# Performance work log

Hardware: AMD Instinct MI355X
Metric: run time of the kernel (lower is better)

Reference implementation:

```python
import jax, jax.numpy as jnp
import numpy as np

D_MODEL = 1024
H = 16
D_K = D_MODEL // H


def setup_inputs() -> dict:
    key = jax.random.key(0)
    ks = jax.random.split(key, 12)
    B, S = 4, 2048
    s = 1.0 / np.sqrt(D_MODEL)
    return {
        "Q": jax.random.normal(ks[0], (B, S, D_MODEL), jnp.float32),
        "K": jax.random.normal(ks[1], (B, S, D_MODEL), jnp.float32),
        "V": jax.random.normal(ks[2], (B, S, D_MODEL), jnp.float32),
        "attn_mask": jnp.ones((B, S), jnp.int32),
        "Wq": jax.random.normal(ks[3], (D_MODEL, D_MODEL), jnp.float32) * s,
        "bq": jax.random.normal(ks[4], (D_MODEL,), jnp.float32) * s,
        "Wk": jax.random.normal(ks[5], (D_MODEL, D_MODEL), jnp.float32) * s,
        "bk": jax.random.normal(ks[6], (D_MODEL,), jnp.float32) * s,
        "Wv": jax.random.normal(ks[7], (D_MODEL, D_MODEL), jnp.float32) * s,
        "bv": jax.random.normal(ks[8], (D_MODEL,), jnp.float32) * s,
        "Wo": jax.random.normal(ks[9], (D_MODEL, D_MODEL), jnp.float32) * s,
        "bo": jax.random.normal(ks[10], (D_MODEL,), jnp.float32) * s,
    }


def _split_heads(x):
    B, S, _ = x.shape
    return x.reshape(B, S, H, D_K).transpose(0, 2, 1, 3)  # (B,H,S,Dk)


def reference(Q, K, V, attn_mask, Wq, bq, Wk, bk, Wv, bv, Wo, bo):
    # Linear projections (torch Linear: x @ W.T + b)
    q = _split_heads(Q @ Wq.T + bq)
    k = _split_heads(K @ Wk.T + bk)
    v = _split_heads(V @ Wv.T + bv)
    scale = 1.0 / jnp.sqrt(jnp.asarray(D_K, q.dtype))
    scores = jnp.einsum("bhqd,bhkd->bhqk", q, k) * scale  # (B,H,S,S)
    # 2-D mask (B,S) broadcast over heads and query positions; 0 -> -inf
    mask = attn_mask[:, None, None, :]
    scores = jnp.where(mask == 0, -jnp.inf, scores)
    attn = jax.nn.softmax(scores, axis=-1)
    # dropout_proba = 0.0 -> identity
    x = jnp.einsum("bhqk,bhkd->bhqd", attn, v)
    B, _, S, _ = x.shape
    x = x.transpose(0, 2, 1, 3).reshape(B, S, D_MODEL)
    return x @ Wo.T + bo
```

## Files before the change

### kernel.cpp

```cpp
#include <hip/hip_runtime.h>
#include <stdint.h>

typedef unsigned short u16;
typedef __attribute__((ext_vector_type(8))) unsigned short u16x8;
typedef __attribute__((ext_vector_type(4))) unsigned short u16x4;
typedef __attribute__((ext_vector_type(2))) __fp16 h16x2;
typedef __attribute__((ext_vector_type(4))) _Float16 f16x4;
typedef __attribute__((ext_vector_type(8))) _Float16 f16x8;
typedef __attribute__((ext_vector_type(4))) float f32x4;

#define MFMA16F16(a,b,c)  __builtin_amdgcn_mfma_f32_16x16x16f16((a),(b),(c),0,0,0)
#define MFMA32F16(a,b,c)  __builtin_amdgcn_mfma_f32_16x16x32_f16((a),(b),(c),0,0,0)

__device__ __forceinline__ f32x4 f4zero() {
    f32x4 z; z[0]=0.f; z[1]=0.f; z[2]=0.f; z[3]=0.f; return z;
}
__device__ __forceinline__ u16x8 cvth8(float4 a, float4 b) {
    union { h16x2 h[4]; u16x8 u; } U;
    U.h[0] = __builtin_amdgcn_cvt_pkrtz(a.x, a.y);
    U.h[1] = __builtin_amdgcn_cvt_pkrtz(a.z, a.w);
    U.h[2] = __builtin_amdgcn_cvt_pkrtz(b.x, b.y);
    U.h[3] = __builtin_amdgcn_cvt_pkrtz(b.z, b.w);
    return U.u;
}

#define GLDS(gp, lp) __builtin_amdgcn_global_load_lds( \
    (const __attribute__((address_space(1))) void*)(gp), \
    (__attribute__((address_space(3))) void*)(lp), 16, 0, 0)

#define QSC 0.1803368801111601f

__global__ __launch_bounds__(256) void conv_all(
    const float* __restrict__ w0, const float* __restrict__ w1,
    const float* __restrict__ w2, const float* __restrict__ w3,
    const float* __restrict__ x0, const float* __restrict__ x1,
    const float* __restrict__ x2,
    u16* __restrict__ wout, u16* __restrict__ xout)
{
    int bx = blockIdx.x;
    const float* src; u16* dst;
    if (bx < 1024) {
        const int t = bx >> 8;
        src = (t == 0) ? w0 : (t == 1) ? w1 : (t == 2) ? w2 : w3;
        const size_t idx = (size_t)(bx & 255) * 4096 + (size_t)threadIdx.x * 16;
        src += idx;
        dst = wout + (size_t)t * 1048576 + idx;
    } else {
        bx -= 1024;
        const int t = bx >> 11;
        src = (t == 0) ? x0 : (t == 1) ? x1 : x2;
        const size_t idx = (size_t)(bx & 2047) * 4096 + (size_t)threadIdx.x * 16;
        src += idx;
        dst = xout + (size_t)t * 8388608 + idx;
    }
    float4 a0 = *(const float4*)(src);
    float4 a1 = *(const float4*)(src + 4);
    float4 a2 = *(const float4*)(src + 8);
    float4 a3 = *(const float4*)(src + 12);
    *(u16x8*)dst       = cvth8(a0, a1);
    *(u16x8*)(dst + 8) = cvth8(a2, a3);
}

__global__ __launch_bounds__(256) void conv_w(
    const float* __restrict__ w0, const float* __restrict__ w1,
    const float* __restrict__ w2, const float* __restrict__ w3,
    u16* __restrict__ out)
{
    const int t = blockIdx.x >> 8;
    const float* src = (t == 0) ? w0 : (t == 1) ? w1 : (t == 2) ? w2 : w3;
    const size_t idx = (size_t)(blockIdx.x & 255) * 4096 + (size_t)threadIdx.x * 16;
    u16* dst = out + (size_t)t * 1048576 + idx;
    float4 a0 = *(const float4*)(src + idx);
    float4 a1 = *(const float4*)(src + idx + 4);
    float4 a2 = *(const float4*)(src + idx + 8);
    float4 a3 = *(const float4*)(src + idx + 12);
    *(u16x8*)dst       = cvth8(a0, a1);
    *(u16x8*)(dst + 8) = cvth8(a2, a3);
}

template<int MODE>
__global__ __launch_bounds__(256, 3) void gemm_qkv(
    const float* __restrict__ Qf, const float* __restrict__ Kf, const float* __restrict__ Vf,
    const u16* __restrict__ xc, const u16* __restrict__ wc,
    const float* __restrict__ Wqf, const float* __restrict__ Wkf, const float* __restrict__ Wvf,
    const float* __restrict__ bq, const float* __restrict__ bk, const float* __restrict__ bv,
    u16* __restrict__ qhp, u16* __restrict__ khp, u16* __restrict__ vtp)
{
    __shared__ __align__(16) char smem[34816];
    u16* As = (u16*)smem;
    u16* Bs = As + 8192;
    u16* Ct = (u16*)smem;

    const int t  = blockIdx.y >> 3;
    const int n0 = (blockIdx.y & 7) * 128;
    const int m0 = blockIdx.x * 128;
    const float* X    = (t == 0) ? Qf : (t == 1) ? Kf : Vf;
    const float* Wf   = (t == 0) ? Wqf : (t == 1) ? Wkf : Wvf;
    const float* bias = (t == 0) ? bq : (t == 1) ? bk : bv;
    const u16*   Wb   = wc + (size_t)t * 1048576;
    const u16*   Xc   = xc + (size_t)t * 8388608;
    u16*         dst  = (t == 0) ? qhp : (t == 1) ? khp : vtp;
    const float  scl  = (t == 0) ? QSC : 1.0f;

    const int tid  = threadIdx.x;
    const int wave = tid >> 6, lane = tid & 63;
    const int quad = lane >> 4, l16 = lane & 15;
    const int wm = (wave >> 1) * 64, wn = (wave & 1) * 64;

    const int grow = lane >> 3;
    const size_t gsw = (size_t)(((lane & 7) ^ grow) << 3);
    const int sr = tid >> 1, hh = tid & 1;
    const size_t xrow = (size_t)(m0 + sr) * 1024;
    const size_t wrow = (size_t)(n0 + sr) * 1024;

    f32x4 acc[4][4];
    for (int i = 0; i < 4; i++) for (int j = 0; j < 4; j++) acc[i][j] = f4zero();

    for (int k0 = 0; k0 < 1024; k0 += 64) {
        if (MODE == 2) {
#pragma unroll
            for (int r = 0; r < 4; r++) {
                const int row = wave * 32 + r * 8 + grow;
                GLDS(Xc + (size_t)(m0 + row) * 1024 + k0 + gsw, As + wave * 2048 + r * 512);
            }
        } else {
#pragma unroll
            for (int c = 0; c < 4; c++) {
                const int ch = hh * 4 + c;
                float4 a0 = *(const float4*)(X + xrow + k0 + ch * 8);
                float4 a1 = *(const float4*)(X + xrow + k0 + ch * 8 + 4);
                *(u16x8*)(As + sr * 64 + ((ch ^ (sr & 7)) << 3)) = cvth8(a0, a1);
            }
        }
        if (MODE >= 1) {
#pragma unroll
            for (int r = 0; r < 4; r++) {
                const int row = wave * 32 + r * 8 + grow;
                GLDS(Wb + (size_t)(n0 + row) * 1024 + k0 + gsw, Bs + wave * 2048 + r * 512);
            }
        } else {
#pragma unroll
            for (int c = 0; c < 4; c++) {
                const int ch = hh * 4 + c;
                float4 b0 = *(const float4*)(Wf + wrow + k0 + ch * 8);
                float4 b1 = *(const float4*)(Wf + wrow + k0 + ch * 8 + 4);
                *(u16x8*)(Bs + sr * 64 + ((ch ^ (sr & 7)) << 3)) = cvth8(b0, b1);
            }
        }
        __syncthreads();

#pragma unroll
        for (int kk = 0; kk < 2; kk++) {
            f16x8 af[4], bfr[4];
#pragma unroll
            for (int i = 0; i < 4; i++) {
                const int ra = wm + i * 16 + l16, rb = wn + i * 16 + l16;
                af[i]  = *(const f16x8*)(As + ra * 64 + (((kk * 4 + quad) ^ (ra & 7)) << 3));
                bfr[i] = *(const f16x8*)(Bs + rb * 64 + (((kk * 4 + quad) ^ (rb & 7)) << 3));
            }
#pragma unroll
            for (int i = 0; i < 4; i++)
#pragma unroll
                for (int j = 0; j < 4; j++)
                    acc[i][j] = MFMA32F16(af[i], bfr[j], acc[i][j]);
        }
        __syncthreads();
    }

#pragma unroll
    for (int i = 0; i < 4; i++) {
        const int row = wm + i * 16 + quad * 4;
#pragma unroll
        for (int j = 0; j < 4; j++) {
            const int col = wn + j * 16 + l16;
            const float bv2 = bias[n0 + col];
#pragma unroll
            for (int r = 0; r < 2; r++) {
                union { h16x2 h; unsigned u; } P;
                P.h = __builtin_amdgcn_cvt_pkrtz((acc[i][j][2*r] + bv2) * scl,
                                                 (acc[i][j][2*r+1] + bv2) * scl);
                Ct[(row + 2*r)     * 136 + col] = (u16)(P.u & 0xFFFF);
                Ct[(row + 2*r + 1) * 136 + col] = (u16)(P.u >> 16);
            }
        }
    }
    __syncthreads();

    if (t < 2) {
        const int row = tid >> 1, half = tid & 1;
        const int m = m0 + row, b = m >> 11, s = m & 2047;
        const int h = (n0 >> 6) + half;
        u16* o = dst + ((size_t)(b * 16 + h) * 2048 + s) * 64;
        const u16* src = Ct + row * 136 + half * 64;
#pragma unroll
        for (int j = 0; j < 64; j += 8) *(u16x8*)(o + j) = *(const u16x8*)(src + j);
    } else {
        const int col = tid >> 1, shalf = tid & 1;
        const int h = (n0 >> 6) + (col >> 6), d = col & 63;
        const int mb = m0 + shalf * 64, b = mb >> 11, sb = mb & 2047;
        u16* o = dst + (size_t)((b * 16 + h) * 64 + d) * 2048 + sb;
#pragma unroll
        for (int j0 = 0; j0 < 64; j0 += 8) {
            u16x8 tv;
#pragma unroll
            for (int j = 0; j < 8; j++) tv[j] = Ct[(shalf * 64 + j0 + j) * 136 + col];
            *(u16x8*)(o + j0) = tv;
        }
    }
}

template<bool WGLDS>
__global__ __launch_bounds__(256, 3) void gemm_o(
    const u16* __restrict__ Xb, const u16* __restrict__ wcO,
    const float* __restrict__ Wf, const float* __restrict__ bias,
    float* __restrict__ out)
{
    __shared__ __align__(16) u16 As[8192];
    __shared__ __align__(16) u16 Bs[8192];

    const int tid  = threadIdx.x;
    const int wave = tid >> 6, lane = tid & 63;
    const int quad = lane >> 4, l16 = lane & 15;
    const int m0 = blockIdx.x * 128, n0 = blockIdx.y * 128;
    const int wm = (wave >> 1) * 64, wn = (wave & 1) * 64;

    const int grow = lane >> 3;
    const size_t gsw = (size_t)(((lane & 7) ^ grow) << 3);
    const int sr = tid >> 1, hh = tid & 1;
    const size_t wrow = (size_t)(n0 + sr) * 1024;

    f32x4 acc[4][4];
    for (int i = 0; i < 4; i++) for (int j = 0; j < 4; j++) acc[i][j] = f4zero();

    for (int k0 = 0; k0 < 1024; k0 += 64) {
#pragma unroll
        for (int r = 0; r < 4; r++) {
            const int row = wave * 32 + r * 8 + grow;
            GLDS(Xb + (size_t)(m0 + row) * 1024 + k0 + gsw, As + wave * 2048 + r * 512);
        }
        if (WGLDS) {
#pragma unroll
            for (int r = 0; r < 4; r++) {
                const int row = wave * 32 + r * 8 + grow;
                GLDS(wcO + (size_t)(n0 + row) * 1024 + k0 + gsw, Bs + wave * 2048 + r * 512);
            }
        } else {
#pragma unroll
            for (int c = 0; c < 4; c++) {
                const int ch = hh * 4 + c;
                float4 b0 = *(const float4*)(Wf + wrow + k0 + ch * 8);
                float4 b1 = *(const float4*)(Wf + wrow + k0 + ch * 8 + 4);
                *(u16x8*)(Bs + sr * 64 + ((ch ^ (sr & 7)) << 3)) = cvth8(b0, b1);
            }
        }
        __syncthreads();

#pragma unroll
        for (int kk = 0; kk < 2; kk++) {
            f16x8 af[4], bfr[4];
#pragma unroll
            for (int i = 0; i < 4; i++) {
                const int ra = wm + i * 16 + l16, rb = wn + i * 16 + l16;
                af[i]  = *(const f16x8*)(As + ra * 64 + (((kk * 4 + quad) ^ (ra & 7)) << 3));
                bfr[i] = *(const f16x8*)(Bs + rb * 64 + (((kk * 4 + quad) ^ (rb & 7)) << 3));
            }
#pragma unroll
            for (int i = 0; i < 4; i++)
#pragma unroll
                for (int j = 0; j < 4; j++)
                    acc[i][j] = MFMA32F16(af[i], bfr[j], acc[i][j]);
        }
        __syncthreads();
    }

#pragma unroll
    for (int i = 0; i < 4; i++)
#pragma unroll
        for (int j = 0; j < 4; j++) {
            const int col = wn + j * 16 + l16;
            const float bv = bias[n0 + col];
#pragma unroll
            for (int r = 0; r < 4; r++)
                out[(size_t)(m0 + wm + i * 16 + quad * 4 + r) * 1024 + n0 + col] = acc[i][j][r] + bv;
        }
}

__global__ __launch_bounds__(256, 4) void attn_fused(
    const u16* __restrict__ qh, const u16* __restrict__ kh,
    const u16* __restrict__ vth, const int* __restrict__ mask,
    u16* __restrict__ xout)
{
    __shared__ __align__(16) u16 Ksh[2][4096];
    __shared__ __align__(16) u16 Vsh[2][4352];
    __shared__ float mshf[2][64];

    const int tid = threadIdx.x, wave = tid >> 6, lane = tid & 63;
    const int quad = lane >> 4, l16 = lane & 15;

    const int flat = blockIdx.x + (blockIdx.y << 4);
    const int xr = flat & 7, xc_ = flat >> 3;
    const int qb = xc_ & 15, bh = xr + ((xc_ >> 4) << 3);
    const int b = bh >> 4, h = bh & 15;
    const int wq = qb * 128 + wave * 32;

    f16x8 qf[2][2];
#pragma unroll
    for (int qg = 0; qg < 2; qg++)
#pragma unroll
        for (int kc = 0; kc < 2; kc++)
            qf[qg][kc] = *(const f16x8*)(qh + ((size_t)bh * 2048 + wq + qg * 16 + l16) * 64
                                         + kc * 32 + quad * 8);

    f32x4 o[2][4];
#pragma unroll
    for (int qg = 0; qg < 2; qg++)
        for (int dt = 0; dt < 4; dt++) o[qg][dt] = f4zero();
    f32x4 lacc[2]; lacc[0] = f4zero(); lacc[1] = f4zero();
    f16x4 ones;
    ones[0] = (_Float16)1.f; ones[1] = (_Float16)1.f;
    ones[2] = (_Float16)1.f; ones[3] = (_Float16)1.f;

    const int klr = lane >> 3;
    const size_t kgoff = (size_t)((lane & 7) ^ klr) << 3;
    const u16* kgb = kh + (size_t)bh * 2048 * 64;

    const int skey = tid >> 2, sc = (tid & 3) * 16;
    const u16* vg = vth + ((size_t)bh * 64 + skey) * 2048 + sc;
    const int mrow = b * 2048;

    {
        GLDS(kgb + (size_t)(wave * 16 + klr) * 64 + kgoff,     &Ksh[0][wave * 1024]);
        GLDS(kgb + (size_t)(wave * 16 + 8 + klr) * 64 + kgoff, &Ksh[0][wave * 1024 + 512]);
        const u16x8 v0 = *(const u16x8*)(vg);
        const u16x8 v1 = *(const u16x8*)(vg + 8);
        u16* vd = &Vsh[0][skey * 68 + sc];
        *(u16x4*)(vd)      = (u16x4){v0[0], v0[1], v0[2], v0[3]};
        *(u16x4*)(vd + 4)  = (u16x4){v0[4], v0[5], v0[6], v0[7]};
        *(u16x4*)(vd + 8)  = (u16x4){v1[0], v1[1], v1[2], v1[3]};
        *(u16x4*)(vd + 12) = (u16x4){v1[4], v1[5], v1[6], v1[7]};
        if (tid < 64) mshf[0][tid] = mask[mrow + tid] ? -10.0f : -1.0e30f;
    }
    __syncthreads();

    for (int t = 0; t < 32; ++t) {
        const int cur = t & 1;
        const u16* Kc = &Ksh[cur][0];
        const u16* Vc = &Vsh[cur][0];

        u16x8 v0, v1; int mreg = 1;
        const int kk2 = (t + 1) * 64;
        if (t < 31) {
            GLDS(kgb + (size_t)(kk2 + wave * 16 + klr) * 64 + kgoff,
                 &Ksh[cur ^ 1][wave * 1024]);
            GLDS(kgb + (size_t)(kk2 + wave * 16 + 8 + klr) * 64 + kgoff,
                 &Ksh[cur ^ 1][wave * 1024 + 512]);
            v0 = *(const u16x8*)(vg + kk2);
            v1 = *(const u16x8*)(vg + kk2 + 8);
            if (tid < 64) mreg = mask[mrow + kk2 + tid];
        }

        __builtin_amdgcn_s_setprio(1);
#pragma unroll
        for (int nt = 0; nt < 4; nt++) {
            const int kro = (nt * 16 + l16) * 64;
            const f16x8 kf0 = *(const f16x8*)(Kc + kro + ((quad ^ (l16 & 7)) << 3));
            const f16x8 kf1 = *(const f16x8*)(Kc + kro + (((quad ^ 4) ^ (l16 & 7)) << 3));
            const float4 mb = *(const float4*)(&mshf[cur][nt * 16 + quad * 4]);
            f16x4 pf[2];
#pragma unroll
            for (int qg = 0; qg < 2; qg++) {
                f32x4 z;
                z[0] = mb.x; z[1] = mb.y; z[2] = mb.z; z[3] = mb.w;
                z = MFMA32F16(kf0, qf[qg][0], z);
                z = MFMA32F16(kf1, qf[qg][1], z);
                union { h16x2 h[2]; f16x4 v; } U;
                U.h[0] = __builtin_amdgcn_cvt_pkrtz(__builtin_amdgcn_exp2f(z[0]),
                                                    __builtin_amdgcn_exp2f(z[1]));
                U.h[1] = __builtin_amdgcn_cvt_pkrtz(__builtin_amdgcn_exp2f(z[2]),
                                                    __builtin_amdgcn_exp2f(z[3]));
                pf[qg] = U.v;
            }
            lacc[0] = MFMA16F16(ones, pf[0], lacc[0]);
            lacc[1] = MFMA16F16(ones, pf[1], lacc[1]);
#pragma unroll
            for (int dt = 0; dt < 4; dt++) {
                const f16x4 vf = *(const f16x4*)(Vc + (dt * 16 + l16) * 68 + nt * 16 + quad * 4);
                o[0][dt] = MFMA16F16(vf, pf[0], o[0][dt]);
                o[1][dt] = MFMA16F16(vf, pf[1], o[1][dt]);
            }
        }
        __builtin_amdgcn_s_setprio(0);

        if (t < 31) {
            u16* vd = &Vsh[cur ^ 1][skey * 68 + sc];
            *(u16x4*)(vd)      = (u16x4){v0[0], v0[1], v0[2], v0[3]};
            *(u16x4*)(vd + 4)  = (u16x4){v0[4], v0[5], v0[6], v0[7]};
            *(u16x4*)(vd + 8)  = (u16x4){v1[0], v1[1], v1[2], v1[3]};
            *(u16x4*)(vd + 12) = (u16x4){v1[4], v1[5], v1[6], v1[7]};
            if (tid < 64) mshf[cur ^ 1][tid] = mreg ? -10.0f : -1.0e30f;
        }
        __syncthreads();
    }

#pragma unroll
    for (int qg = 0; qg < 2; qg++) {
        const float inv = 1.0f / lacc[qg][0];
        const int row = wq + qg * 16 + l16;
        u16* op = xout + ((size_t)b * 2048 + row) * 1024 + h * 64;
#pragma unroll
        for (int dt = 0; dt < 4; dt++) {
            union { h16x2 h[2]; u16x4 u; } U;
            U.h[0] = __builtin_amdgcn_cvt_pkrtz(o[qg][dt][0] * inv, o[qg][dt][1] * inv);
            U.h[1] = __builtin_amdgcn_cvt_pkrtz(o[qg][dt][2] * inv, o[qg][dt][3] * inv);
            *(u16x4*)(op + dt * 16 + quad * 4) = U.u;
        }
    }
}

extern "C" void kernel_launch(void* const* d_in, const int* in_sizes, int n_in,
                              void* d_out, int out_size, void* d_ws, size_t ws_size,
                              hipStream_t stream)
{
    const float* Q   = (const float*)d_in[0];
    const float* K   = (const float*)d_in[1];
    const float* V   = (const float*)d_in[2];
    const int*   msk = (const int*)d_in[3];
    const float* Wq  = (const float*)d_in[4];
    const float* bq  = (const float*)d_in[5];
    const float* Wk  = (const float*)d_in[6];
    const float* bk  = (const float*)d_in[7];
    const float* Wv  = (const float*)d_in[8];
    const float* bv  = (const float*)d_in[9];
    const float* Wo  = (const float*)d_in[10];
    const float* bo  = (const float*)d_in[11];

    u16* base = (u16*)d_ws;
    dim3 blk(256);
    dim3 gq(64, 24);
    dim3 ga(16, 64);
    dim3 go(64, 8);

    if (ws_size >= 109051904UL) {
        u16* wc  = base;
        u16* xc  = base + 4194304;
        u16* qhp = xc + 25165824;
        u16* khp = qhp + 8388608;
        u16* vtp = khp + 8388608;
        u16* xs  = xc;
        conv_all<<<7168, blk, 0, stream>>>(Wq, Wk, Wv, Wo, Q, K, V, wc, xc);
        gemm_qkv<2><<<gq, blk, 0, stream>>>(Q, K, V, xc, wc,
            nullptr, nullptr, nullptr, bq, bk, bv, qhp, khp, vtp);
        attn_fused<<<ga, blk, 0, stream>>>(qhp, khp, vtp, msk, xs);
        gemm_o<true><<<go, blk, 0, stream>>>(xs, wc + 3 * 1048576, nullptr, bo, (float*)d_out);
    } else if (ws_size >= ((size_t)72 << 20)) {
        u16* wc  = base;
        u16* qhp = base + 4194304;
        u16* khp = qhp + 8388608;
        u16* vtp = khp + 8388608;
        u16* xs  = vtp + 8388608;
        conv_w<<<1024, blk, 0, stream>>>(Wq, Wk, Wv, Wo, wc);
        gemm_qkv<1><<<gq, blk, 0, stream>>>(Q, K, V, nullptr, wc,
            nullptr, nullptr, nullptr, bq, bk, bv, qhp, khp, vtp);
        attn_fused<<<ga, blk, 0, stream>>>(qhp, khp, vtp, msk, xs);
        gemm_o<true><<<go, blk, 0, stream>>>(xs, wc + 3 * 1048576, nullptr, bo, (float*)d_out);
    } else {
        u16* qhp = base;
        u16* khp = qhp + 8388608;
        u16* vtp = khp + 8388608;
        u16* xs  = vtp + 8388608;
        gemm_qkv<0><<<gq, blk, 0, stream>>>(Q, K, V, nullptr, nullptr,
            Wq, Wk, Wv, bq, bk, bv, qhp, khp, vtp);
        attn_fused<<<ga, blk, 0, stream>>>(qhp, khp, vtp, msk, xs);
        gemm_o<false><<<go, blk, 0, stream>>>(xs, nullptr, Wo, bo, (float*)d_out);
    }
}
```

Measured before the change: 357.4 us.

## Triple-buffer QKV and output GEMMs with async global-to-LDS prefetch

Both projection GEMMs switch from a single-buffered K=64 loop with two barriers per step to a three-stage ring of K=32 LDS tiles. Each step issues direct global-to-LDS loads two tiles ahead, then waits on counted vmcnt with one barrier per step, so memory latency can overlap the MFMA work. MFMA sections are also raised in wave priority. The cost is that the XOR swizzle is dropped (a 32-wide unpadded LDS layout that may cause bank conflicts), LDS use grows to 48KB per block, and the pipeline relies on hand-written waitcnt counts.

```diff
diff --git a/kernel.cpp b/kernel.cpp
--- a/kernel.cpp
+++ b/kernel.cpp
@@ -86,10 +86,8 @@
     const float* __restrict__ bq, const float* __restrict__ bk, const float* __restrict__ bv,
     u16* __restrict__ qhp, u16* __restrict__ khp, u16* __restrict__ vtp)
 {
-    __shared__ __align__(16) char smem[34816];
-    u16* As = (u16*)smem;
-    u16* Bs = As + 8192;
-    u16* Ct = (u16*)smem;
+    __shared__ __align__(16) u16 smem[24576];
+    u16* Ct = smem;
 
     const int t  = blockIdx.y >> 3;
     const int n0 = (blockIdx.y & 7) * 128;
@@ -107,65 +105,94 @@
     const int quad = lane >> 4, l16 = lane & 15;
     const int wm = (wave >> 1) * 64, wn = (wave & 1) * 64;
 
-    const int grow = lane >> 3;
-    const size_t gsw = (size_t)(((lane & 7) ^ grow) << 3);
+    const int srow = lane >> 2;
+    const size_t scol = (size_t)(lane & 3) * 8;
     const int sr = tid >> 1, hh = tid & 1;
-    const size_t xrow = (size_t)(m0 + sr) * 1024;
-    const size_t wrow = (size_t)(n0 + sr) * 1024;
 
     f32x4 acc[4][4];
     for (int i = 0; i < 4; i++) for (int j = 0; j < 4; j++) acc[i][j] = f4zero();
 
-    for (int k0 = 0; k0 < 1024; k0 += 64) {
-        if (MODE == 2) {
-#pragma unroll
-            for (int r = 0; r < 4; r++) {
-                const int row = wave * 32 + r * 8 + grow;
-                GLDS(Xc + (size_t)(m0 + row) * 1024 + k0 + gsw, As + wave * 2048 + r * 512);
+    auto stageA = [&](int b, int kt) {
+        GLDS(Xc + (size_t)(m0 + wave * 32 +      srow) * 1024 + kt * 32 + scol,
+             smem + b * 8192 + wave * 1024);
+        GLDS(Xc + (size_t)(m0 + wave * 32 + 16 + srow) * 1024 + kt * 32 + scol,
+             smem + b * 8192 + wave * 1024 + 512);
+    };
+    auto stageB = [&](int b, int kt) {
+        GLDS(Wb + (size_t)(n0 + wave * 32 +      srow) * 1024 + kt * 32 + scol,
+             smem + b * 8192 + 4096 + wave * 1024);
+        GLDS(Wb + (size_t)(n0 + wave * 32 + 16 + srow) * 1024 + kt * 32 + scol,
+             smem + b * 8192 + 4096 + wave * 1024 + 512);
+    };
+    float4 xr_[4];
+    auto loadX = [&](int kt) {
+        const float* p = X + (size_t)(m0 + sr) * 1024 + kt * 32 + hh * 16;
+        xr_[0] = *(const float4*)(p);     xr_[1] = *(const float4*)(p + 4);
+        xr_[2] = *(const float4*)(p + 8); xr_[3] = *(const float4*)(p + 12);
+    };
+    auto writeX = [&](int b) {
+        u16* d = smem + b * 8192 + sr * 32 + hh * 16;
+        *(u16x8*)d       = cvth8(xr_[0], xr_[1]);
+        *(u16x8*)(d + 8) = cvth8(xr_[2], xr_[3]);
+    };
+    auto comp = [&](int b) {
+        const u16* As = smem + b * 8192;
+        const u16* Bs = As + 4096;
+        f16x8 af[4], bfr[4];
+#pragma unroll
+        for (int i = 0; i < 4; i++) {
+            af[i]  = *(const f16x8*)(As + (wm + i * 16 + l16) * 32 + quad * 8);
+            bfr[i] = *(const f16x8*)(Bs + (wn + i * 16 + l16) * 32 + quad * 8);
+        }
+        __builtin_amdgcn_s_setprio(1);
+#pragma unroll
+        for (int i = 0; i < 4; i++)
+#pragma unroll
+            for (int j = 0; j < 4; j++)
+                acc[i][j] = MFMA32F16(af[i], bfr[j], acc[i][j]);
+        __builtin_amdgcn_s_setprio(0);
+    };
+
+    if (MODE == 0) {
+        for (int kt = 0; kt < 32; ++kt) {
+            loadX(kt); writeX(0);
+            const float* p = Wf + (size_t)(n0 + sr) * 1024 + kt * 32 + hh * 16;
+            float4 b0 = *(const float4*)(p);     float4 b1 = *(const float4*)(p + 4);
+            float4 b2 = *(const float4*)(p + 8); float4 b3 = *(const float4*)(p + 12);
+            u16* d = smem + 4096 + sr * 32 + hh * 16;
+            *(u16x8*)d       = cvth8(b0, b1);
+            *(u16x8*)(d + 8) = cvth8(b2, b3);
+            __syncthreads();
+            comp(0);
+            __syncthreads();
+        }
+    } else {
+        if (MODE == 2) stageA(0, 0);
+        stageB(0, 0);
+        if (MODE == 2) stageA(1, 1);
+        stageB(1, 1);
+        if (MODE == 1) { loadX(0); writeX(0); }
+        int bA = 0, bB = 1, bC = 2;
+        for (int kt = 0; kt < 31; ++kt) {
+            if (MODE == 2) asm volatile("s_waitcnt vmcnt(4) lgkmcnt(0)" ::: "memory");
+            else           asm volatile("s_waitcnt vmcnt(2) lgkmcnt(0)" ::: "memory");
+            __builtin_amdgcn_s_barrier();
+            __builtin_amdgcn_sched_barrier(0);
+            if (MODE == 1) loadX(kt + 1);
+            if (kt < 30) {
+                if (MODE == 2) stageA(bC, kt + 2);
+                stageB(bC, kt + 2);
             }
-        } else {
-#pragma unroll
-            for (int c = 0; c < 4; c++) {
-                const int ch = hh * 4 + c;
-                float4 a0 = *(const float4*)(X + xrow + k0 + ch * 8);
-                float4 a1 = *(const float4*)(X + xrow + k0 + ch * 8 + 4);
-                *(u16x8*)(As + sr * 64 + ((ch ^ (sr & 7)) << 3)) = cvth8(a0, a1);
-            }
-        }
-        if (MODE >= 1) {
-#pragma unroll
-            for (int r = 0; r < 4; r++) {
-                const int row = wave * 32 + r * 8 + grow;
-                GLDS(Wb + (size_t)(n0 + row) * 1024 + k0 + gsw, Bs + wave * 2048 + r * 512);
-            }
-        } else {
-#pragma unroll
-            for (int c = 0; c < 4; c++) {
-                const int ch = hh * 4 + c;
-                float4 b0 = *(const float4*)(Wf + wrow + k0 + ch * 8);
-                float4 b1 = *(const float4*)(Wf + wrow + k0 + ch * 8 + 4);
-                *(u16x8*)(Bs + sr * 64 + ((ch ^ (sr & 7)) << 3)) = cvth8(b0, b1);
-            }
-        }
-        __syncthreads();
-
-#pragma unroll
-        for (int kk = 0; kk < 2; kk++) {
-            f16x8 af[4], bfr[4];
-#pragma unroll
-            for (int i = 0; i < 4; i++) {
-                const int ra = wm + i * 16 + l16, rb = wn + i * 16 + l16;
-                af[i]  = *(const f16x8*)(As + ra * 64 + (((kk * 4 + quad) ^ (ra & 7)) << 3));
-                bfr[i] = *(const f16x8*)(Bs + rb * 64 + (((kk * 4 + quad) ^ (rb & 7)) << 3));
-            }
-#pragma unroll
-            for (int i = 0; i < 4; i++)
-#pragma unroll
-                for (int j = 0; j < 4; j++)
-                    acc[i][j] = MFMA32F16(af[i], bfr[j], acc[i][j]);
-        }
-        __syncthreads();
-    }
+            comp(bA);
+            if (MODE == 1) writeX(bB);
+            int tmp = bA; bA = bB; bB = bC; bC = tmp;
+        }
+        asm volatile("s_waitcnt vmcnt(0) lgkmcnt(0)" ::: "memory");
+        __builtin_amdgcn_s_barrier();
+        __builtin_amdgcn_sched_barrier(0);
+        comp(bA);
+    }
+    __syncthreads();
 
 #pragma unroll
     for (int i = 0; i < 4; i++) {
@@ -209,14 +236,13 @@
     }
 }
 
-template<bool WGLDS>
+template<int MODE>
 __global__ __launch_bounds__(256, 3) void gemm_o(
     const u16* __restrict__ Xb, const u16* __restrict__ wcO,
     const float* __restrict__ Wf, const float* __restrict__ bias,
     float* __restrict__ out)
 {
-    __shared__ __align__(16) u16 As[8192];
-    __shared__ __align__(16) u16 Bs[8192];
+    __shared__ __align__(16) u16 smem[24576];
 
     const int tid  = threadIdx.x;
     const int wave = tid >> 6, lane = tid & 63;
@@ -224,54 +250,78 @@
     const int m0 = blockIdx.x * 128, n0 = blockIdx.y * 128;
     const int wm = (wave >> 1) * 64, wn = (wave & 1) * 64;
 
-    const int grow = lane >> 3;
-    const size_t gsw = (size_t)(((lane & 7) ^ grow) << 3);
+    const int srow = lane >> 2;
+    const size_t scol = (size_t)(lane & 3) * 8;
     const int sr = tid >> 1, hh = tid & 1;
-    const size_t wrow = (size_t)(n0 + sr) * 1024;
 
     f32x4 acc[4][4];
     for (int i = 0; i < 4; i++) for (int j = 0; j < 4; j++) acc[i][j] = f4zero();
 
-    for (int k0 = 0; k0 < 1024; k0 += 64) {
-#pragma unroll
-        for (int r = 0; r < 4; r++) {
-            const int row = wave * 32 + r * 8 + grow;
-            GLDS(Xb + (size_t)(m0 + row) * 1024 + k0 + gsw, As + wave * 2048 + r * 512);
-        }
-        if (WGLDS) {
-#pragma unroll
-            for (int r = 0; r < 4; r++) {
-                const int row = wave * 32 + r * 8 + grow;
-                GLDS(wcO + (size_t)(n0 + row) * 1024 + k0 + gsw, Bs + wave * 2048 + r * 512);
-            }
-        } else {
-#pragma unroll
-            for (int c = 0; c < 4; c++) {
-                const int ch = hh * 4 + c;
-                float4 b0 = *(const float4*)(Wf + wrow + k0 + ch * 8);
-                float4 b1 = *(const float4*)(Wf + wrow + k0 + ch * 8 + 4);
-                *(u16x8*)(Bs + sr * 64 + ((ch ^ (sr & 7)) << 3)) = cvth8(b0, b1);
-            }
-        }
-        __syncthreads();
-
-#pragma unroll
-        for (int kk = 0; kk < 2; kk++) {
-            f16x8 af[4], bfr[4];
-#pragma unroll
-            for (int i = 0; i < 4; i++) {
-                const int ra = wm + i * 16 + l16, rb = wn + i * 16 + l16;
-                af[i]  = *(const f16x8*)(As + ra * 64 + (((kk * 4 + quad) ^ (ra & 7)) << 3));
-                bfr[i] = *(const f16x8*)(Bs + rb * 64 + (((kk * 4 + quad) ^ (rb & 7)) << 3));
-            }
-#pragma unroll
-            for (int i = 0; i < 4; i++)
-#pragma unroll
-                for (int j = 0; j < 4; j++)
-                    acc[i][j] = MFMA32F16(af[i], bfr[j], acc[i][j]);
-        }
-        __syncthreads();
-    }
+    auto stageA = [&](int b, int kt) {
+        GLDS(Xb + (size_t)(m0 + wave * 32 +      srow) * 1024 + kt * 32 + scol,
+             smem + b * 8192 + wave * 1024);
+        GLDS(Xb + (size_t)(m0 + wave * 32 + 16 + srow) * 1024 + kt * 32 + scol,
+             smem + b * 8192 + wave * 1024 + 512);
+    };
+    auto stageB = [&](int b, int kt) {
+        GLDS(wcO + (size_t)(n0 + wave * 32 +      srow) * 1024 + kt * 32 + scol,
+             smem + b * 8192 + 4096 + wave * 1024);
+        GLDS(wcO + (size_t)(n0 + wave * 32 + 16 + srow) * 1024 + kt * 32 + scol,
+             smem + b * 8192 + 4096 + wave * 1024 + 512);
+    };
+    float4 wr_[4];
+    auto loadW = [&](int kt) {
+        const float* p = Wf + (size_t)(n0 + sr) * 1024 + kt * 32 + hh * 16;
+        wr_[0] = *(const float4*)(p);     wr_[1] = *(const float4*)(p + 4);
+        wr_[2] = *(const float4*)(p + 8); wr_[3] = *(const float4*)(p + 12);
+    };
+    auto writeW = [&](int b) {
+        u16* d = smem + b * 8192 + 4096 + sr * 32 + hh * 16;
+        *(u16x8*)d       = cvth8(wr_[0], wr_[1]);
+        *(u16x8*)(d + 8) = cvth8(wr_[2], wr_[3]);
+    };
+    auto comp = [&](int b) {
+        const u16* As = smem + b * 8192;
+        const u16* Bs = As + 4096;
+        f16x8 af[4], bfr[4];
+#pragma unroll
+        for (int i = 0; i < 4; i++) {
+            af[i]  = *(const f16x8*)(As + (wm + i * 16 + l16) * 32 + quad * 8);
+            bfr[i] = *(const f16x8*)(Bs + (wn + i * 16 + l16) * 32 + quad * 8);
+        }
+        __builtin_amdgcn_s_setprio(1);
+#pragma unroll
+        for (int i = 0; i < 4; i++)
+#pragma unroll
+            for (int j = 0; j < 4; j++)
+                acc[i][j] = MFMA32F16(af[i], bfr[j], acc[i][j]);
+        __builtin_amdgcn_s_setprio(0);
+    };
+
+    stageA(0, 0);
+    if (MODE == 2) stageB(0, 0);
+    stageA(1, 1);
+    if (MODE == 2) stageB(1, 1);
+    if (MODE == 1) { loadW(0); writeW(0); }
+    int bA = 0, bB = 1, bC = 2;
+    for (int kt = 0; kt < 31; ++kt) {
+        if (MODE == 2) asm volatile("s_waitcnt vmcnt(4) lgkmcnt(0)" ::: "memory");
+        else           asm volatile("s_waitcnt vmcnt(2) lgkmcnt(0)" ::: "memory");
+        __builtin_amdgcn_s_barrier();
+        __builtin_amdgcn_sched_barrier(0);
+        if (MODE == 1) loadW(kt + 1);
+        if (kt < 30) {
+            stageA(bC, kt + 2);
+            if (MODE == 2) stageB(bC, kt + 2);
+        }
+        comp(bA);
+        if (MODE == 1) writeW(bB);
+        int tmp = bA; bA = bB; bB = bC; bC = tmp;
+    }
+    asm volatile("s_waitcnt vmcnt(0) lgkmcnt(0)" ::: "memory");
+    __builtin_amdgcn_s_barrier();
+    __builtin_amdgcn_sched_barrier(0);
+    comp(bA);
 
 #pragma unroll
     for (int i = 0; i < 4; i++)
@@ -451,7 +501,7 @@
         gemm_qkv<2><<<gq, blk, 0, stream>>>(Q, K, V, xc, wc,
             nullptr, nullptr, nullptr, bq, bk, bv, qhp, khp, vtp);
         attn_fused<<<ga, blk, 0, stream>>>(qhp, khp, vtp, msk, xs);
-        gemm_o<true><<<go, blk, 0, stream>>>(xs, wc + 3 * 1048576, nullptr, bo, (float*)d_out);
+        gemm_o<2><<<go, blk, 0, stream>>>(xs, wc + 3 * 1048576, nullptr, bo, (float*)d_out);
     } else if (ws_size >= ((size_t)72 << 20)) {
         u16* wc  = base;
         u16* qhp = base + 4194304;
@@ -462,7 +512,7 @@
         gemm_qkv<1><<<gq, blk, 0, stream>>>(Q, K, V, nullptr, wc,
             nullptr, nullptr, nullptr, bq, bk, bv, qhp, khp, vtp);
         attn_fused<<<ga, blk, 0, stream>>>(qhp, khp, vtp, msk, xs);
-        gemm_o<true><<<go, blk, 0, stream>>>(xs, wc + 3 * 1048576, nullptr, bo, (float*)d_out);
+        gemm_o<2><<<go, blk, 0, stream>>>(xs, wc + 3 * 1048576, nullptr, bo, (float*)d_out);
     } else {
         u16* qhp = base;
         u16* khp = qhp + 8388608;
@@ -471,6 +521,6 @@
         gemm_qkv<0><<<gq, blk, 0, stream>>>(Q, K, V, nullptr, nullptr,
             Wq, Wk, Wv, bq, bk, bv, qhp, khp, vtp);
         attn_fused<<<ga, blk, 0, stream>>>(qhp, khp, vtp, msk, xs);
-        gemm_o<false><<<go, blk, 0, stream>>>(xs, nullptr, Wo, bo, (float*)d_out);
-    }
-}
+        gemm_o<1><<<go, blk, 0, stream>>>(xs, nullptr, Wo, bo, (float*)d_out);
+    }
+}
```

Result: faster. 347.7 us (-2.7%).
